# Kernel tuning notes

Measured on AMD Instinct MI355X. Metric: run time of the kernel, lower is better.

## Reference

```python
import jax, jax.numpy as jnp
import numpy as np

GROUP_SIZE = 64  # matches init_kwargs group_size


def setup_inputs() -> dict:
    key = jax.random.key(0)
    k1, k2, k3, k4 = jax.random.split(key, 4)
    B, S, D_in, D_out = 4, 2048, 4096, 4096
    x = jax.random.normal(k1, (B, S, D_in), dtype=jnp.float32)
    # symmetric int8 quantized weights in [-127, 127]
    weight_quant = jax.random.randint(k2, (D_out, D_in), -127, 128, dtype=jnp.int32)
    num_groups = (D_out * D_in) // GROUP_SIZE
    # positive per-group scales (abs_max / 127 of a typical weight group)
    weight_scale = jax.random.uniform(k3, (num_groups,), dtype=jnp.float32,
                                      minval=1e-3, maxval=2e-2)
    bias = jax.random.normal(k4, (D_out,), dtype=jnp.float32) * 0.01
    return {"x": x, "weight_quant": weight_quant,
            "weight_scale": weight_scale, "bias": bias}


def reference(x, weight_quant, weight_scale, bias):
    # Group-wise symmetric dequantization: flatten row-major, scale each
    # contiguous group of GROUP_SIZE elements by its own scale.
    out_f, in_f = weight_quant.shape
    w = weight_quant.astype(jnp.float32).reshape(-1, GROUP_SIZE)  # [num_groups, G]
    w = w * weight_scale[:, None]
    w = w.reshape(out_f, in_f).astype(x.dtype)
    # F.linear(x, W, b) = x @ W^T + b
    return jnp.einsum('bsi,oi->bso', x, w) + bias
```

## Files before the change

### kernel.cpp

```cpp
#include <hip/hip_runtime.h>
#include <stdint.h>


typedef __attribute__((ext_vector_type(8))) short short8;
typedef __attribute__((ext_vector_type(8))) unsigned short ushort8;
typedef __attribute__((ext_vector_type(4))) float f32x4;
typedef __attribute__((ext_vector_type(16))) float f32x16;
typedef __attribute__((ext_vector_type(4))) float float4v;
typedef __attribute__((ext_vector_type(4))) int int4v;

typedef __attribute__((address_space(1))) void g_void;
typedef __attribute__((address_space(3))) void l_void;

__device__ __forceinline__ unsigned short f2bf(float f) {
  union { float f; unsigned int u; } v; v.f = f;
  unsigned int r = v.u + 0x7FFFu + ((v.u >> 16) & 1u);
  return (unsigned short)(r >> 16);
}

__device__ __forceinline__ void async_copy16(const void* g, void* l) {
  __builtin_amdgcn_global_load_lds((const g_void*)g, (l_void*)l, 16, 0, 0);
}

__device__ __forceinline__ void wg_barrier() {
  asm volatile("" ::: "memory");
  __builtin_amdgcn_s_barrier();
  asm volatile("" ::: "memory");
}

#define WAIT_VMCNT(N) asm volatile("s_waitcnt vmcnt(" #N ")" ::: "memory")

__global__ __launch_bounds__(256) void cvt_kernel(
    const float* __restrict__ x, const int* __restrict__ w,
    const float* __restrict__ s, unsigned short* __restrict__ ox,
    unsigned short* __restrict__ ow, int n8x, int n8w, int gx) {
  if ((int)blockIdx.x < gx) {
    int t = blockIdx.x * 256 + threadIdx.x;
    if (t >= n8x) return;
    const float4v* xp = (const float4v*)x + (size_t)t * 2;
    float4v a = xp[0], b = xp[1];
    ushort8 r;
    r[0] = f2bf(a[0]); r[1] = f2bf(a[1]); r[2] = f2bf(a[2]); r[3] = f2bf(a[3]);
    r[4] = f2bf(b[0]); r[5] = f2bf(b[1]); r[6] = f2bf(b[2]); r[7] = f2bf(b[3]);
    *(ushort8*)(ox + (size_t)t * 8) = r;
  } else {
    int t = ((int)blockIdx.x - gx) * 256 + threadIdx.x;
    if (t >= n8w) return;
    const int4v* wp = (const int4v*)w + (size_t)t * 2;
    int4v q0 = wp[0], q1 = wp[1];
    float sc = s[t >> 3];
    ushort8 r;
    r[0] = f2bf((float)q0[0] * sc); r[1] = f2bf((float)q0[1] * sc);
    r[2] = f2bf((float)q0[2] * sc); r[3] = f2bf((float)q0[3] * sc);
    r[4] = f2bf((float)q1[0] * sc); r[5] = f2bf((float)q1[1] * sc);
    r[6] = f2bf((float)q1[2] * sc); r[7] = f2bf((float)q1[3] * sc);
    *(ushort8*)(ow + (size_t)t * 8) = r;
  }
}


#define MF(a, b, c) __builtin_amdgcn_mfma_f32_16x16x32_bf16(a, b, c, 0, 0, 0)

#define LDA(base, mh) do {                              \
    const unsigned char* _p = (base) + aoff + (mh) * 4096; \
    av0 = *(const short8*)(_p);                         \
    av1 = *(const short8*)(_p + 1024);                  \
    av2 = *(const short8*)(_p + 2048);                  \
    av3 = *(const short8*)(_p + 3072);                  \
  } while (0)

#define LDB(base) do {                                  \
    const unsigned char* _p = (base) + boff;            \
    bv0 = *(const short8*)(_p);                         \
    bv1 = *(const short8*)(_p + 1024);                  \
    bv2 = *(const short8*)(_p + 2048);                  \
    bv3 = *(const short8*)(_p + 3072);                  \
  } while (0)

#define MM16(mb) do {                                           \
    acc[(mb)+0][0] = MF(av0, bv0, acc[(mb)+0][0]);              \
    acc[(mb)+0][1] = MF(av0, bv1, acc[(mb)+0][1]);              \
    acc[(mb)+0][2] = MF(av0, bv2, acc[(mb)+0][2]);              \
    acc[(mb)+0][3] = MF(av0, bv3, acc[(mb)+0][3]);              \
    acc[(mb)+1][0] = MF(av1, bv0, acc[(mb)+1][0]);              \
    acc[(mb)+1][1] = MF(av1, bv1, acc[(mb)+1][1]);              \
    acc[(mb)+1][2] = MF(av1, bv2, acc[(mb)+1][2]);              \
    acc[(mb)+1][3] = MF(av1, bv3, acc[(mb)+1][3]);              \
    acc[(mb)+2][0] = MF(av2, bv0, acc[(mb)+2][0]);              \
    acc[(mb)+2][1] = MF(av2, bv1, acc[(mb)+2][1]);              \
    acc[(mb)+2][2] = MF(av2, bv2, acc[(mb)+2][2]);              \
    acc[(mb)+2][3] = MF(av2, bv3, acc[(mb)+2][3]);              \
    acc[(mb)+3][0] = MF(av3, bv0, acc[(mb)+3][0]);              \
    acc[(mb)+3][1] = MF(av3, bv1, acc[(mb)+3][1]);              \
    acc[(mb)+3][2] = MF(av3, bv2, acc[(mb)+3][2]);              \
    acc[(mb)+3][3] = MF(av3, bv3, acc[(mb)+3][3]);              \
  } while (0)

#define PRIO1 __builtin_amdgcn_s_setprio(1)
#define PRIO0 __builtin_amdgcn_s_setprio(0)

__device__ __forceinline__ void stage2(const unsigned short* src, int rstride,
                                       unsigned char* dst) {
  async_copy16(src, dst);
  async_copy16(src + rstride, dst + 8192);
}

__global__ __launch_bounds__(512, 2) void gemm_8p(
    const unsigned short* __restrict__ Xb,
    const unsigned short* __restrict__ Wb,
    const float* __restrict__ bias,
    float* __restrict__ C, int M, int N, int K) {
  __shared__ __align__(16) unsigned char smem[131072];
  const int tid = threadIdx.x;
  const int lane = tid & 63, w = tid >> 6;
  const int wm = w >> 2, wn = w & 3;
  const int l15 = lane & 15;

  const int nbn = N >> 8;
  int bid = blockIdx.x;
  {
    const int nwg = gridDim.x;
    if ((nwg & 7) == 0) bid = (bid & 7) * (nwg >> 3) + (bid >> 3);
  }
  const int m0 = (bid / nbn) << 8;
  const int n0 = (bid % nbn) << 8;

  const int chnk = (((lane >> 4) ^ ((l15 >> 1) & 3)) << 4);
  const int aoff = (wm * 128 + l15) * 64 + chnk;
  const int boff = (wn * 64 + l15) * 64 + chnk;

  const int rl = tid >> 2;
  const int lc = (tid & 3) ^ ((tid >> 3) & 3);
  const unsigned short* pA = Xb + (size_t)(m0 + rl) * K + lc * 8;
  const unsigned short* pB = Wb + (size_t)(n0 + rl) * K + lc * 8;
  const int rstride = K << 7;
  const int wuo = w << 10;

  f32x4 acc[8][4];
#pragma unroll
  for (int i = 0; i < 8; i++)
#pragma unroll
    for (int j = 0; j < 4; j++) acc[i][j] = (f32x4)(0.f);

  const int NT = K >> 6;

  stage2(pA, rstride, smem + wuo);
  stage2(pB, rstride, smem + 65536 + wuo);
  stage2(pA + 32, rstride, smem + 16384 + wuo);
  stage2(pB + 32, rstride, smem + 65536 + 16384 + wuo);
  WAIT_VMCNT(4);
  wg_barrier();

  short8 av0, av1, av2, av3, bv0, bv1, bv2, bv3;

  for (int t = 0; t < NT - 1; ++t) {
    const int p = t & 1;
    const unsigned char* Ab = smem + p * 32768;
    const unsigned char* Bb = smem + 65536 + p * 32768;
    unsigned char* Aq = smem + (p ^ 1) * 32768 + wuo;
    unsigned char* Bq = smem + 65536 + (p ^ 1) * 32768 + wuo;
    const unsigned short* sA = pA + (size_t)(t + 1) * 64;
    const unsigned short* sB = pB + (size_t)(t + 1) * 64;

    LDA(Ab, 0); LDB(Bb);
    stage2(sA, rstride, Aq);
    wg_barrier();
    PRIO1; MM16(0); PRIO0;
    wg_barrier();
    LDA(Ab, 1);
    stage2(sB, rstride, Bq);
    wg_barrier();
    PRIO1; MM16(4); PRIO0;
    WAIT_VMCNT(4);
    wg_barrier();
    LDA(Ab + 16384, 0); LDB(Bb + 16384);
    stage2(sA + 32, rstride, Aq + 16384);
    wg_barrier();
    PRIO1; MM16(0); PRIO0;
    wg_barrier();
    LDA(Ab + 16384, 1);
    stage2(sB + 32, rstride, Bq + 16384);
    wg_barrier();
    PRIO1; MM16(4); PRIO0;
    WAIT_VMCNT(4);
    wg_barrier();
  }

  {
    const int p = (NT - 1) & 1;
    const unsigned char* Ab = smem + p * 32768;
    const unsigned char* Bb = smem + 65536 + p * 32768;
    LDA(Ab, 0); LDB(Bb);
    wg_barrier();
    PRIO1; MM16(0); PRIO0;
    wg_barrier();
    LDA(Ab, 1);
    wg_barrier();
    PRIO1; MM16(4); PRIO0;
    WAIT_VMCNT(0);
    wg_barrier();
    LDA(Ab + 16384, 0); LDB(Bb + 16384);
    wg_barrier();
    PRIO1; MM16(0); PRIO0;
    wg_barrier();
    LDA(Ab + 16384, 1);
    wg_barrier();
    PRIO1; MM16(4); PRIO0;
  }

  const int gm = m0 + wm * 128 + ((lane >> 4) << 2);
  const int gn = n0 + wn * 64 + l15;
  float bvs[4];
#pragma unroll
  for (int g = 0; g < 4; ++g) bvs[g] = bias[gn + g * 16];
#pragma unroll
  for (int mf = 0; mf < 8; ++mf) {
    const size_t rb = (size_t)(gm + mf * 16) * N + gn;
#pragma unroll
    for (int r = 0; r < 4; ++r) {
#pragma unroll
      for (int g = 0; g < 4; ++g)
        C[rb + (size_t)r * N + g * 16] = acc[mf][g][r] + bvs[g];
    }
  }
}

#define BM 128
#define BN 128
#define BK 64

__global__ __launch_bounds__(256) void gemm_fused(
    const float* __restrict__ Xf, const int* __restrict__ Wq,
    const float* __restrict__ Ws, const float* __restrict__ bias,
    float* __restrict__ C, int M, int N, int K) {
  __shared__ unsigned char smem[(BM * BK + BN * BK) * 2];
  const int tid = threadIdx.x;
  const int lane = tid & 63, wid = tid >> 6;
  const int m0 = blockIdx.y * BM, n0 = blockIdx.x * BN;
  const int sr = lane >> 3, fc = (lane & 7) ^ sr;
  const int arow = m0 + wid * 32 + sr, brow = n0 + wid * 32 + sr;
  unsigned char* As = smem;
  unsigned char* Bs = smem + BM * BK * 2;
  unsigned char* stA = As + wid * 4096 + lane * 16;
  unsigned char* stB = Bs + wid * 4096 + lane * 16;
  const int l31 = lane & 31, lh = lane >> 5, le = lane & 7;
  const int wm = (wid & 1) * 64, wn = (wid >> 1) * 64;
  const unsigned char* Aw = As + (wm + l31) * 128;
  const unsigned char* Bw = Bs + (wn + l31) * 128;
  const int Kg = K >> 6;

  f32x16 acc[2][2];
#pragma unroll
  for (int i = 0; i < 2; i++)
#pragma unroll
    for (int j = 0; j < 2; j++) acc[i][j] = (f32x16)(0.f);

  for (int k0 = 0; k0 < K; k0 += BK) {
#pragma unroll
    for (int t = 0; t < 4; t++) {
      const float4v* xa = (const float4v*)(Xf + (size_t)(arow + t * 8) * K + k0 + fc * 8);
      float4v x0 = xa[0], x1 = xa[1];
      ushort8 ra;
      ra[0] = f2bf(x0[0]); ra[1] = f2bf(x0[1]); ra[2] = f2bf(x0[2]); ra[3] = f2bf(x0[3]);
      ra[4] = f2bf(x1[0]); ra[5] = f2bf(x1[1]); ra[6] = f2bf(x1[2]); ra[7] = f2bf(x1[3]);
      *(ushort8*)(stA + t * 1024) = ra;
      const int4v* wq = (const int4v*)(Wq + (size_t)(brow + t * 8) * K + k0 + fc * 8);
      int4v q0 = wq[0], q1 = wq[1];
      float sc = Ws[(size_t)(brow + t * 8) * Kg + (k0 >> 6)];
      ushort8 rb;
      rb[0] = f2bf((float)q0[0] * sc); rb[1] = f2bf((float)q0[1] * sc);
      rb[2] = f2bf((float)q0[2] * sc); rb[3] = f2bf((float)q0[3] * sc);
      rb[4] = f2bf((float)q1[0] * sc); rb[5] = f2bf((float)q1[1] * sc);
      rb[6] = f2bf((float)q1[2] * sc); rb[7] = f2bf((float)q1[3] * sc);
      *(ushort8*)(stB + t * 1024) = rb;
    }
    __syncthreads();
#pragma unroll
    for (int s = 0; s < 4; s++) {
      const int off = ((s + 4 * lh) ^ le) << 4;
      short8 a0 = *(const short8*)(Aw + off);
      short8 a1 = *(const short8*)(Aw + 4096 + off);
      short8 b0 = *(const short8*)(Bw + off);
      short8 b1 = *(const short8*)(Bw + 4096 + off);
      acc[0][0] = __builtin_amdgcn_mfma_f32_32x32x16_bf16(a0, b0, acc[0][0], 0, 0, 0);
      acc[0][1] = __builtin_amdgcn_mfma_f32_32x32x16_bf16(a0, b1, acc[0][1], 0, 0, 0);
      acc[1][0] = __builtin_amdgcn_mfma_f32_32x32x16_bf16(a1, b0, acc[1][0], 0, 0, 0);
      acc[1][1] = __builtin_amdgcn_mfma_f32_32x32x16_bf16(a1, b1, acc[1][1], 0, 0, 0);
    }
    __syncthreads();
  }

  const int gm = m0 + wm + 4 * lh, gn = n0 + wn + l31;
#pragma unroll
  for (int j = 0; j < 2; j++) {
    const int col = gn + j * 32;
    const float bv = bias[col];
#pragma unroll
    for (int i = 0; i < 2; i++) {
      const int rbase = gm + i * 32;
      f32x16 v = acc[i][j];
#pragma unroll
      for (int r = 0; r < 16; r++) {
        const int row = rbase + (r & 3) + 8 * (r >> 2);
        C[(size_t)row * N + col] = v[r] + bv;
      }
    }
  }
}

extern "C" void kernel_launch(void* const* d_in, const int* in_sizes, int n_in,
                              void* d_out, int out_size, void* d_ws, size_t ws_size,
                              hipStream_t stream) {
  const float* x = (const float*)d_in[0];
  const int* wq = (const int*)d_in[1];
  const float* wsc = (const float*)d_in[2];
  const float* bias = (const float*)d_in[3];
  float* out = (float*)d_out;

  const int N = in_sizes[3];
  const int K = in_sizes[1] / N;
  const int M = in_sizes[0] / K;

  const size_t needX = (size_t)M * K * 2;
  const size_t needW = (size_t)N * K * 2;
  const bool big = (M % 256 == 0) && (N % 256 == 0) && (K % 64 == 0) && (K >= 128);

  if (big && ws_size >= needX + needW) {
    unsigned short* Xb = (unsigned short*)d_ws;
    unsigned short* Wb = (unsigned short*)((char*)d_ws + needX);
    const int n8x = (M * K) / 8, n8w = (N * K) / 8;
    const int gx = (n8x + 255) / 256, gw = (n8w + 255) / 256;
    cvt_kernel<<<gx + gw, 256, 0, stream>>>(x, wq, wsc, Xb, Wb, n8x, n8w, gx);
    dim3 grid((M / 256) * (N / 256));
    gemm_8p<<<grid, 512, 0, stream>>>(Xb, Wb, bias, out, M, N, K);
  } else {
    dim3 grid(N / BN, M / BM), block(256);
    gemm_fused<<<grid, block, 0, stream>>>(x, wq, wsc, bias, out, M, N, K);
  }
}
```

Before: 500.6 us.

## Switch GEMM to 32x32x16 MFMA, fewer barriers, grid-stride convert kernel

The main GEMM now uses 32x32x16 bf16 MFMA tiles in place of 16x16x32, with a new LDS read pattern and swizzle. Each K-half loads all of its operands in one batch, and all four async stages are issued up front, which removes half of the workgroup barriers per iteration. The conversion kernel becomes a grid-stride loop over a fixed grid of 1376+688 blocks rather than one block per chunk. The larger MFMA halves the number of instructions and cuts LDS read traffic per flop. In exchange, the epilogue stores become less coalesced and the new wait counts and swizzle must be exactly right.

Result: slower. 579.8 us (+15.8%).

```diff
diff --git a/kernel.cpp b/kernel.cpp
--- a/kernel.cpp
+++ b/kernel.cpp
@@ -35,65 +35,68 @@
     const float* __restrict__ s, unsigned short* __restrict__ ox,
     unsigned short* __restrict__ ow, int n8x, int n8w, int gx) {
   if ((int)blockIdx.x < gx) {
-    int t = blockIdx.x * 256 + threadIdx.x;
-    if (t >= n8x) return;
-    const float4v* xp = (const float4v*)x + (size_t)t * 2;
-    float4v a = xp[0], b = xp[1];
-    ushort8 r;
-    r[0] = f2bf(a[0]); r[1] = f2bf(a[1]); r[2] = f2bf(a[2]); r[3] = f2bf(a[3]);
-    r[4] = f2bf(b[0]); r[5] = f2bf(b[1]); r[6] = f2bf(b[2]); r[7] = f2bf(b[3]);
-    *(ushort8*)(ox + (size_t)t * 8) = r;
+    const int stride = gx * 256;
+    for (int t = blockIdx.x * 256 + threadIdx.x; t < n8x; t += stride) {
+      const float4v* xp = (const float4v*)x + (size_t)t * 2;
+      float4v a = xp[0], b = xp[1];
+      ushort8 r;
+      r[0] = f2bf(a[0]); r[1] = f2bf(a[1]); r[2] = f2bf(a[2]); r[3] = f2bf(a[3]);
+      r[4] = f2bf(b[0]); r[5] = f2bf(b[1]); r[6] = f2bf(b[2]); r[7] = f2bf(b[3]);
+      *(ushort8*)(ox + (size_t)t * 8) = r;
+    }
   } else {
-    int t = ((int)blockIdx.x - gx) * 256 + threadIdx.x;
-    if (t >= n8w) return;
-    const int4v* wp = (const int4v*)w + (size_t)t * 2;
-    int4v q0 = wp[0], q1 = wp[1];
-    float sc = s[t >> 3];
-    ushort8 r;
-    r[0] = f2bf((float)q0[0] * sc); r[1] = f2bf((float)q0[1] * sc);
-    r[2] = f2bf((float)q0[2] * sc); r[3] = f2bf((float)q0[3] * sc);
-    r[4] = f2bf((float)q1[0] * sc); r[5] = f2bf((float)q1[1] * sc);
-    r[6] = f2bf((float)q1[2] * sc); r[7] = f2bf((float)q1[3] * sc);
-    *(ushort8*)(ow + (size_t)t * 8) = r;
-  }
-}
-
-
-#define MF(a, b, c) __builtin_amdgcn_mfma_f32_16x16x32_bf16(a, b, c, 0, 0, 0)
-
-#define LDA(base, mh) do {                              \
-    const unsigned char* _p = (base) + aoff + (mh) * 4096; \
-    av0 = *(const short8*)(_p);                         \
-    av1 = *(const short8*)(_p + 1024);                  \
-    av2 = *(const short8*)(_p + 2048);                  \
-    av3 = *(const short8*)(_p + 3072);                  \
+    const int stride = ((int)gridDim.x - gx) * 256;
+    for (int t = ((int)blockIdx.x - gx) * 256 + threadIdx.x; t < n8w; t += stride) {
+      const int4v* wp = (const int4v*)w + (size_t)t * 2;
+      int4v q0 = wp[0], q1 = wp[1];
+      float sc = s[t >> 3];
+      ushort8 r;
+      r[0] = f2bf((float)q0[0] * sc); r[1] = f2bf((float)q0[1] * sc);
+      r[2] = f2bf((float)q0[2] * sc); r[3] = f2bf((float)q0[3] * sc);
+      r[4] = f2bf((float)q1[0] * sc); r[5] = f2bf((float)q1[1] * sc);
+      r[6] = f2bf((float)q1[2] * sc); r[7] = f2bf((float)q1[3] * sc);
+      *(ushort8*)(ow + (size_t)t * 8) = r;
+    }
+  }
+}
+
+
+#define MF32(a, b, c) __builtin_amdgcn_mfma_f32_32x32x16_bf16(a, b, c, 0, 0, 0)
+
+#define READ12(AU, BU) do {                              \
+    const unsigned char* _a = (AU) + abase;              \
+    const unsigned char* _b = (BU) + bbase;              \
+    a00 = *(const short8*)(_a + ca0);                    \
+    a10 = *(const short8*)(_a + 2048 + ca0);             \
+    a20 = *(const short8*)(_a + 4096 + ca0);             \
+    a30 = *(const short8*)(_a + 6144 + ca0);             \
+    a01 = *(const short8*)(_a + ca1);                    \
+    a11 = *(const short8*)(_a + 2048 + ca1);             \
+    a21 = *(const short8*)(_a + 4096 + ca1);             \
+    a31 = *(const short8*)(_a + 6144 + ca1);             \
+    b00 = *(const short8*)(_b + ca0);                    \
+    b10 = *(const short8*)(_b + 2048 + ca0);             \
+    b01 = *(const short8*)(_b + ca1);                    \
+    b11 = *(const short8*)(_b + 2048 + ca1);             \
   } while (0)
 
-#define LDB(base) do {                                  \
-    const unsigned char* _p = (base) + boff;            \
-    bv0 = *(const short8*)(_p);                         \
-    bv1 = *(const short8*)(_p + 1024);                  \
-    bv2 = *(const short8*)(_p + 2048);                  \
-    bv3 = *(const short8*)(_p + 3072);                  \
-  } while (0)
-
-#define MM16(mb) do {                                           \
-    acc[(mb)+0][0] = MF(av0, bv0, acc[(mb)+0][0]);              \
-    acc[(mb)+0][1] = MF(av0, bv1, acc[(mb)+0][1]);              \
-    acc[(mb)+0][2] = MF(av0, bv2, acc[(mb)+0][2]);              \
-    acc[(mb)+0][3] = MF(av0, bv3, acc[(mb)+0][3]);              \
-    acc[(mb)+1][0] = MF(av1, bv0, acc[(mb)+1][0]);              \
-    acc[(mb)+1][1] = MF(av1, bv1, acc[(mb)+1][1]);              \
-    acc[(mb)+1][2] = MF(av1, bv2, acc[(mb)+1][2]);              \
-    acc[(mb)+1][3] = MF(av1, bv3, acc[(mb)+1][3]);              \
-    acc[(mb)+2][0] = MF(av2, bv0, acc[(mb)+2][0]);              \
-    acc[(mb)+2][1] = MF(av2, bv1, acc[(mb)+2][1]);              \
-    acc[(mb)+2][2] = MF(av2, bv2, acc[(mb)+2][2]);              \
-    acc[(mb)+2][3] = MF(av2, bv3, acc[(mb)+2][3]);              \
-    acc[(mb)+3][0] = MF(av3, bv0, acc[(mb)+3][0]);              \
-    acc[(mb)+3][1] = MF(av3, bv1, acc[(mb)+3][1]);              \
-    acc[(mb)+3][2] = MF(av3, bv2, acc[(mb)+3][2]);              \
-    acc[(mb)+3][3] = MF(av3, bv3, acc[(mb)+3][3]);              \
+#define MFMA16() do {                                    \
+    acc[0][0] = MF32(a00, b00, acc[0][0]);               \
+    acc[1][0] = MF32(a10, b00, acc[1][0]);               \
+    acc[2][0] = MF32(a20, b00, acc[2][0]);               \
+    acc[3][0] = MF32(a30, b00, acc[3][0]);               \
+    acc[0][1] = MF32(a00, b10, acc[0][1]);               \
+    acc[1][1] = MF32(a10, b10, acc[1][1]);               \
+    acc[2][1] = MF32(a20, b10, acc[2][1]);               \
+    acc[3][1] = MF32(a30, b10, acc[3][1]);               \
+    acc[0][0] = MF32(a01, b01, acc[0][0]);               \
+    acc[1][0] = MF32(a11, b01, acc[1][0]);               \
+    acc[2][0] = MF32(a21, b01, acc[2][0]);               \
+    acc[3][0] = MF32(a31, b01, acc[3][0]);               \
+    acc[0][1] = MF32(a01, b11, acc[0][1]);               \
+    acc[1][1] = MF32(a11, b11, acc[1][1]);               \
+    acc[2][1] = MF32(a21, b11, acc[2][1]);               \
+    acc[3][1] = MF32(a31, b11, acc[3][1]);               \
   } while (0)
 
 #define PRIO1 __builtin_amdgcn_s_setprio(1)
@@ -114,7 +117,7 @@
   const int tid = threadIdx.x;
   const int lane = tid & 63, w = tid >> 6;
   const int wm = w >> 2, wn = w & 3;
-  const int l15 = lane & 15;
+  const int l31 = lane & 31, kg = lane >> 5;
 
   const int nbn = N >> 8;
   int bid = blockIdx.x;
@@ -125,9 +128,11 @@
   const int m0 = (bid / nbn) << 8;
   const int n0 = (bid % nbn) << 8;
 
-  const int chnk = (((lane >> 4) ^ ((l15 >> 1) & 3)) << 4);
-  const int aoff = (wm * 128 + l15) * 64 + chnk;
-  const int boff = (wn * 64 + l15) * 64 + chnk;
+  const int xr = (l31 >> 1) & 3;
+  const int ca0 = ((0 + kg) ^ xr) << 4;
+  const int ca1 = ((2 + kg) ^ xr) << 4;
+  const int abase = (wm * 128 + l31) * 64;
+  const int bbase = (wn * 64 + l31) * 64;
 
   const int rl = tid >> 2;
   const int lc = (tid & 3) ^ ((tid >> 3) & 3);
@@ -136,11 +141,11 @@
   const int rstride = K << 7;
   const int wuo = w << 10;
 
-  f32x4 acc[8][4];
-#pragma unroll
-  for (int i = 0; i < 8; i++)
-#pragma unroll
-    for (int j = 0; j < 4; j++) acc[i][j] = (f32x4)(0.f);
+  f32x16 acc[4][2];
+#pragma unroll
+  for (int i = 0; i < 4; i++)
+#pragma unroll
+    for (int j = 0; j < 2; j++) acc[i][j] = (f32x16)(0.f);
 
   const int NT = K >> 6;
 
@@ -151,76 +156,62 @@
   WAIT_VMCNT(4);
   wg_barrier();
 
-  short8 av0, av1, av2, av3, bv0, bv1, bv2, bv3;
+  short8 a00, a10, a20, a30, a01, a11, a21, a31, b00, b10, b01, b11;
 
   for (int t = 0; t < NT - 1; ++t) {
     const int p = t & 1;
-    const unsigned char* Ab = smem + p * 32768;
-    const unsigned char* Bb = smem + 65536 + p * 32768;
+    const unsigned char* Au = smem + p * 32768;
+    const unsigned char* Bu = smem + 65536 + p * 32768;
     unsigned char* Aq = smem + (p ^ 1) * 32768 + wuo;
     unsigned char* Bq = smem + 65536 + (p ^ 1) * 32768 + wuo;
     const unsigned short* sA = pA + (size_t)(t + 1) * 64;
     const unsigned short* sB = pB + (size_t)(t + 1) * 64;
 
-    LDA(Ab, 0); LDB(Bb);
+    READ12(Au, Bu);
     stage2(sA, rstride, Aq);
-    wg_barrier();
-    PRIO1; MM16(0); PRIO0;
-    wg_barrier();
-    LDA(Ab, 1);
     stage2(sB, rstride, Bq);
-    wg_barrier();
-    PRIO1; MM16(4); PRIO0;
-    WAIT_VMCNT(4);
-    wg_barrier();
-    LDA(Ab + 16384, 0); LDB(Bb + 16384);
     stage2(sA + 32, rstride, Aq + 16384);
-    wg_barrier();
-    PRIO1; MM16(0); PRIO0;
-    wg_barrier();
-    LDA(Ab + 16384, 1);
     stage2(sB + 32, rstride, Bq + 16384);
     wg_barrier();
-    PRIO1; MM16(4); PRIO0;
+    PRIO1; MFMA16(); PRIO0;
+    WAIT_VMCNT(8);
+    wg_barrier();
+    READ12(Au + 16384, Bu + 16384);
+    wg_barrier();
+    PRIO1; MFMA16(); PRIO0;
     WAIT_VMCNT(4);
     wg_barrier();
   }
 
   {
     const int p = (NT - 1) & 1;
-    const unsigned char* Ab = smem + p * 32768;
-    const unsigned char* Bb = smem + 65536 + p * 32768;
-    LDA(Ab, 0); LDB(Bb);
-    wg_barrier();
-    PRIO1; MM16(0); PRIO0;
-    wg_barrier();
-    LDA(Ab, 1);
-    wg_barrier();
-    PRIO1; MM16(4); PRIO0;
+    const unsigned char* Au = smem + p * 32768;
+    const unsigned char* Bu = smem + 65536 + p * 32768;
+    READ12(Au, Bu);
+    wg_barrier();
+    PRIO1; MFMA16(); PRIO0;
     WAIT_VMCNT(0);
     wg_barrier();
-    LDA(Ab + 16384, 0); LDB(Bb + 16384);
-    wg_barrier();
-    PRIO1; MM16(0); PRIO0;
-    wg_barrier();
-    LDA(Ab + 16384, 1);
-    wg_barrier();
-    PRIO1; MM16(4); PRIO0;
-  }
-
-  const int gm = m0 + wm * 128 + ((lane >> 4) << 2);
-  const int gn = n0 + wn * 64 + l15;
-  float bvs[4];
-#pragma unroll
-  for (int g = 0; g < 4; ++g) bvs[g] = bias[gn + g * 16];
-#pragma unroll
-  for (int mf = 0; mf < 8; ++mf) {
-    const size_t rb = (size_t)(gm + mf * 16) * N + gn;
-#pragma unroll
-    for (int r = 0; r < 4; ++r) {
-#pragma unroll
-      for (int g = 0; g < 4; ++g)
-        C[rb + (size_t)r * N + g * 16] = acc[mf][g][r] + bvs[g];
+    READ12(Au + 16384, Bu + 16384);
+    wg_barrier();
+    PRIO1; MFMA16(); PRIO0;
+  }
+
+  const int gm = m0 + wm * 128 + 4 * kg;
+  const int gn = n0 + wn * 64 + l31;
+  const float bv0 = bias[gn], bv1 = bias[gn + 32];
+#pragma unroll
+  for (int mt = 0; mt < 4; ++mt) {
+#pragma unroll
+    for (int nt = 0; nt < 2; ++nt) {
+      const float bv = nt ? bv1 : bv0;
+      const int col = gn + nt * 32;
+      f32x16 v = acc[mt][nt];
+#pragma unroll
+      for (int r = 0; r < 16; ++r) {
+        const int row = gm + mt * 32 + (r & 3) + 8 * (r >> 2);
+        C[(size_t)row * N + col] = v[r] + bv;
+      }
     }
   }
 }
@@ -329,7 +320,7 @@
     unsigned short* Xb = (unsigned short*)d_ws;
     unsigned short* Wb = (unsigned short*)((char*)d_ws + needX);
     const int n8x = (M * K) / 8, n8w = (N * K) / 8;
-    const int gx = (n8x + 255) / 256, gw = (n8w + 255) / 256;
+    const int gx = 1376, gw = 688;
     cvt_kernel<<<gx + gw, 256, 0, stream>>>(x, wq, wsc, Xb, Wb, n8x, n8w, gx);
     dim3 grid((M / 256) * (N / 256));
     gemm_8p<<<grid, 512, 0, stream>>>(Xb, Wb, bias, out, M, N, K);
```

## Shrink GEMM tile to 128x256 with BK32 double buffer and grid-stride convert

Applied to the files above, without the earlier changes.

The main bf16 GEMM now uses 128x256 block tiles with a K-step of 32 and a smaller 48 KB shared buffer. Each wave keeps a 64x64 accumulator, and launch bounds ask for 4 blocks per CU, trading per-block data reuse for higher occupancy and more blocks. The pipeline is simpler: async copy of the next tile, then MFMA on the current one, then a full vmcnt wait and barrier each step, so load latency is less hidden. The conversion kernel becomes grid-stride with fixed block counts to cut launch size.

Result: slower. 540.8 us (+8.0%).

```diff
diff --git a/kernel.cpp b/kernel.cpp
--- a/kernel.cpp
+++ b/kernel.cpp
@@ -35,34 +35,36 @@
     const float* __restrict__ s, unsigned short* __restrict__ ox,
     unsigned short* __restrict__ ow, int n8x, int n8w, int gx) {
   if ((int)blockIdx.x < gx) {
-    int t = blockIdx.x * 256 + threadIdx.x;
-    if (t >= n8x) return;
-    const float4v* xp = (const float4v*)x + (size_t)t * 2;
-    float4v a = xp[0], b = xp[1];
-    ushort8 r;
-    r[0] = f2bf(a[0]); r[1] = f2bf(a[1]); r[2] = f2bf(a[2]); r[3] = f2bf(a[3]);
-    r[4] = f2bf(b[0]); r[5] = f2bf(b[1]); r[6] = f2bf(b[2]); r[7] = f2bf(b[3]);
-    *(ushort8*)(ox + (size_t)t * 8) = r;
+    const int stride = gx * 256;
+    for (int t = blockIdx.x * 256 + threadIdx.x; t < n8x; t += stride) {
+      const float4v* xp = (const float4v*)x + (size_t)t * 2;
+      float4v a = xp[0], b = xp[1];
+      ushort8 r;
+      r[0] = f2bf(a[0]); r[1] = f2bf(a[1]); r[2] = f2bf(a[2]); r[3] = f2bf(a[3]);
+      r[4] = f2bf(b[0]); r[5] = f2bf(b[1]); r[6] = f2bf(b[2]); r[7] = f2bf(b[3]);
+      *(ushort8*)(ox + (size_t)t * 8) = r;
+    }
   } else {
-    int t = ((int)blockIdx.x - gx) * 256 + threadIdx.x;
-    if (t >= n8w) return;
-    const int4v* wp = (const int4v*)w + (size_t)t * 2;
-    int4v q0 = wp[0], q1 = wp[1];
-    float sc = s[t >> 3];
-    ushort8 r;
-    r[0] = f2bf((float)q0[0] * sc); r[1] = f2bf((float)q0[1] * sc);
-    r[2] = f2bf((float)q0[2] * sc); r[3] = f2bf((float)q0[3] * sc);
-    r[4] = f2bf((float)q1[0] * sc); r[5] = f2bf((float)q1[1] * sc);
-    r[6] = f2bf((float)q1[2] * sc); r[7] = f2bf((float)q1[3] * sc);
-    *(ushort8*)(ow + (size_t)t * 8) = r;
-  }
-}
-
-
-#define MF(a, b, c) __builtin_amdgcn_mfma_f32_16x16x32_bf16(a, b, c, 0, 0, 0)
-
-#define LDA(base, mh) do {                              \
-    const unsigned char* _p = (base) + aoff + (mh) * 4096; \
+    const int stride = ((int)gridDim.x - gx) * 256;
+    for (int t = ((int)blockIdx.x - gx) * 256 + threadIdx.x; t < n8w; t += stride) {
+      const int4v* wp = (const int4v*)w + (size_t)t * 2;
+      int4v q0 = wp[0], q1 = wp[1];
+      float sc = s[t >> 3];
+      ushort8 r;
+      r[0] = f2bf((float)q0[0] * sc); r[1] = f2bf((float)q0[1] * sc);
+      r[2] = f2bf((float)q0[2] * sc); r[3] = f2bf((float)q0[3] * sc);
+      r[4] = f2bf((float)q1[0] * sc); r[5] = f2bf((float)q1[1] * sc);
+      r[6] = f2bf((float)q1[2] * sc); r[7] = f2bf((float)q1[3] * sc);
+      *(ushort8*)(ow + (size_t)t * 8) = r;
+    }
+  }
+}
+
+
+#define MF16(a, b, c) __builtin_amdgcn_mfma_f32_16x16x32_bf16(a, b, c, 0, 0, 0)
+
+#define LDA(base) do {                                  \
+    const unsigned char* _p = (base) + aoff;            \
     av0 = *(const short8*)(_p);                         \
     av1 = *(const short8*)(_p + 1024);                  \
     av2 = *(const short8*)(_p + 2048);                  \
@@ -77,23 +79,23 @@
     bv3 = *(const short8*)(_p + 3072);                  \
   } while (0)
 
-#define MM16(mb) do {                                           \
-    acc[(mb)+0][0] = MF(av0, bv0, acc[(mb)+0][0]);              \
-    acc[(mb)+0][1] = MF(av0, bv1, acc[(mb)+0][1]);              \
-    acc[(mb)+0][2] = MF(av0, bv2, acc[(mb)+0][2]);              \
-    acc[(mb)+0][3] = MF(av0, bv3, acc[(mb)+0][3]);              \
-    acc[(mb)+1][0] = MF(av1, bv0, acc[(mb)+1][0]);              \
-    acc[(mb)+1][1] = MF(av1, bv1, acc[(mb)+1][1]);              \
-    acc[(mb)+1][2] = MF(av1, bv2, acc[(mb)+1][2]);              \
-    acc[(mb)+1][3] = MF(av1, bv3, acc[(mb)+1][3]);              \
-    acc[(mb)+2][0] = MF(av2, bv0, acc[(mb)+2][0]);              \
-    acc[(mb)+2][1] = MF(av2, bv1, acc[(mb)+2][1]);              \
-    acc[(mb)+2][2] = MF(av2, bv2, acc[(mb)+2][2]);              \
-    acc[(mb)+2][3] = MF(av2, bv3, acc[(mb)+2][3]);              \
-    acc[(mb)+3][0] = MF(av3, bv0, acc[(mb)+3][0]);              \
-    acc[(mb)+3][1] = MF(av3, bv1, acc[(mb)+3][1]);              \
-    acc[(mb)+3][2] = MF(av3, bv2, acc[(mb)+3][2]);              \
-    acc[(mb)+3][3] = MF(av3, bv3, acc[(mb)+3][3]);              \
+#define MM16() do {                                     \
+    acc[0][0] = MF16(av0, bv0, acc[0][0]);              \
+    acc[0][1] = MF16(av0, bv1, acc[0][1]);              \
+    acc[0][2] = MF16(av0, bv2, acc[0][2]);              \
+    acc[0][3] = MF16(av0, bv3, acc[0][3]);              \
+    acc[1][0] = MF16(av1, bv0, acc[1][0]);              \
+    acc[1][1] = MF16(av1, bv1, acc[1][1]);              \
+    acc[1][2] = MF16(av1, bv2, acc[1][2]);              \
+    acc[1][3] = MF16(av1, bv3, acc[1][3]);              \
+    acc[2][0] = MF16(av2, bv0, acc[2][0]);              \
+    acc[2][1] = MF16(av2, bv1, acc[2][1]);              \
+    acc[2][2] = MF16(av2, bv2, acc[2][2]);              \
+    acc[2][3] = MF16(av2, bv3, acc[2][3]);              \
+    acc[3][0] = MF16(av3, bv0, acc[3][0]);              \
+    acc[3][1] = MF16(av3, bv1, acc[3][1]);              \
+    acc[3][2] = MF16(av3, bv2, acc[3][2]);              \
+    acc[3][3] = MF16(av3, bv3, acc[3][3]);              \
   } while (0)
 
 #define PRIO1 __builtin_amdgcn_s_setprio(1)
@@ -105,12 +107,21 @@
   async_copy16(src + rstride, dst + 8192);
 }
 
-__global__ __launch_bounds__(512, 2) void gemm_8p(
+#define TILE(Au, Bu, Aq, Bq, koff) do {                 \
+    async_copy16(pA + (koff), Aq);                      \
+    stage2(pB + (koff), rstride, Bq);                   \
+    LDA(Au); LDB(Bu);                                   \
+    PRIO1; MM16(); PRIO0;                               \
+    WAIT_VMCNT(0);                                      \
+    wg_barrier();                                       \
+  } while (0)
+
+__global__ __launch_bounds__(512, 4) void gemm_8p(
     const unsigned short* __restrict__ Xb,
     const unsigned short* __restrict__ Wb,
     const float* __restrict__ bias,
     float* __restrict__ C, int M, int N, int K) {
-  __shared__ __align__(16) unsigned char smem[131072];
+  __shared__ __align__(16) unsigned char smem[49152];
   const int tid = threadIdx.x;
   const int lane = tid & 63, w = tid >> 6;
   const int wm = w >> 2, wn = w & 3;
@@ -122,11 +133,11 @@
     const int nwg = gridDim.x;
     if ((nwg & 7) == 0) bid = (bid & 7) * (nwg >> 3) + (bid >> 3);
   }
-  const int m0 = (bid / nbn) << 8;
+  const int m0 = (bid / nbn) << 7;
   const int n0 = (bid % nbn) << 8;
 
   const int chnk = (((lane >> 4) ^ ((l15 >> 1) & 3)) << 4);
-  const int aoff = (wm * 128 + l15) * 64 + chnk;
+  const int aoff = (wm * 64 + l15) * 64 + chnk;
   const int boff = (wn * 64 + l15) * 64 + chnk;
 
   const int rl = tid >> 2;
@@ -136,91 +147,52 @@
   const int rstride = K << 7;
   const int wuo = w << 10;
 
-  f32x4 acc[8][4];
-#pragma unroll
-  for (int i = 0; i < 8; i++)
+  const unsigned char* A0 = smem;
+  const unsigned char* A1 = smem + 8192;
+  const unsigned char* B0 = smem + 16384;
+  const unsigned char* B1 = smem + 32768;
+  unsigned char* A0q = smem + wuo;
+  unsigned char* A1q = smem + 8192 + wuo;
+  unsigned char* B0q = smem + 16384 + wuo;
+  unsigned char* B1q = smem + 32768 + wuo;
+
+  f32x4 acc[4][4];
+#pragma unroll
+  for (int i = 0; i < 4; i++)
 #pragma unroll
     for (int j = 0; j < 4; j++) acc[i][j] = (f32x4)(0.f);
 
-  const int NT = K >> 6;
-
-  stage2(pA, rstride, smem + wuo);
-  stage2(pB, rstride, smem + 65536 + wuo);
-  stage2(pA + 32, rstride, smem + 16384 + wuo);
-  stage2(pB + 32, rstride, smem + 65536 + 16384 + wuo);
-  WAIT_VMCNT(4);
+  const int NT = K >> 5;
+
+  async_copy16(pA, A0q);
+  stage2(pB, rstride, B0q);
+  WAIT_VMCNT(0);
   wg_barrier();
 
   short8 av0, av1, av2, av3, bv0, bv1, bv2, bv3;
 
-  for (int t = 0; t < NT - 1; ++t) {
-    const int p = t & 1;
-    const unsigned char* Ab = smem + p * 32768;
-    const unsigned char* Bb = smem + 65536 + p * 32768;
-    unsigned char* Aq = smem + (p ^ 1) * 32768 + wuo;
-    unsigned char* Bq = smem + 65536 + (p ^ 1) * 32768 + wuo;
-    const unsigned short* sA = pA + (size_t)(t + 1) * 64;
-    const unsigned short* sB = pB + (size_t)(t + 1) * 64;
-
-    LDA(Ab, 0); LDB(Bb);
-    stage2(sA, rstride, Aq);
-    wg_barrier();
-    PRIO1; MM16(0); PRIO0;
-    wg_barrier();
-    LDA(Ab, 1);
-    stage2(sB, rstride, Bq);
-    wg_barrier();
-    PRIO1; MM16(4); PRIO0;
-    WAIT_VMCNT(4);
-    wg_barrier();
-    LDA(Ab + 16384, 0); LDB(Bb + 16384);
-    stage2(sA + 32, rstride, Aq + 16384);
-    wg_barrier();
-    PRIO1; MM16(0); PRIO0;
-    wg_barrier();
-    LDA(Ab + 16384, 1);
-    stage2(sB + 32, rstride, Bq + 16384);
-    wg_barrier();
-    PRIO1; MM16(4); PRIO0;
-    WAIT_VMCNT(4);
-    wg_barrier();
-  }
-
-  {
-    const int p = (NT - 1) & 1;
-    const unsigned char* Ab = smem + p * 32768;
-    const unsigned char* Bb = smem + 65536 + p * 32768;
-    LDA(Ab, 0); LDB(Bb);
-    wg_barrier();
-    PRIO1; MM16(0); PRIO0;
-    wg_barrier();
-    LDA(Ab, 1);
-    wg_barrier();
-    PRIO1; MM16(4); PRIO0;
-    WAIT_VMCNT(0);
-    wg_barrier();
-    LDA(Ab + 16384, 0); LDB(Bb + 16384);
-    wg_barrier();
-    PRIO1; MM16(0); PRIO0;
-    wg_barrier();
-    LDA(Ab + 16384, 1);
-    wg_barrier();
-    PRIO1; MM16(4); PRIO0;
-  }
-
-  const int gm = m0 + wm * 128 + ((lane >> 4) << 2);
+  for (int t2 = 0; t2 < (NT >> 1) - 1; ++t2) {
+    const int koff = t2 * 64 + 32;
+    TILE(A0, B0, A1q, B1q, koff);
+    TILE(A1, B1, A0q, B0q, koff + 32);
+  }
+  TILE(A0, B0, A1q, B1q, (NT - 1) * 32);
+  LDA(A1); LDB(B1);
+  PRIO1; MM16(); PRIO0;
+
+  const int gm = m0 + wm * 64 + ((lane >> 4) << 2);
   const int gn = n0 + wn * 64 + l15;
   float bvs[4];
 #pragma unroll
   for (int g = 0; g < 4; ++g) bvs[g] = bias[gn + g * 16];
 #pragma unroll
-  for (int mf = 0; mf < 8; ++mf) {
-    const size_t rb = (size_t)(gm + mf * 16) * N + gn;
+  for (int mt = 0; mt < 4; ++mt) {
+    const size_t rb = (size_t)(gm + mt * 16) * N + gn;
 #pragma unroll
     for (int r = 0; r < 4; ++r) {
 #pragma unroll
-      for (int g = 0; g < 4; ++g)
-        C[rb + (size_t)r * N + g * 16] = acc[mf][g][r] + bvs[g];
+      for (int nt = 0; nt < 4; ++nt)
+        C[rb + (size_t)r * N + nt * 16] = acc[mt][nt][r] + bvs[nt];
     }
   }
 }
@@ -323,15 +295,15 @@
 
   const size_t needX = (size_t)M * K * 2;
   const size_t needW = (size_t)N * K * 2;
-  const bool big = (M % 256 == 0) && (N % 256 == 0) && (K % 64 == 0) && (K >= 128);
+  const bool big = (M % 128 == 0) && (N % 256 == 0) && (K % 64 == 0) && (K >= 128);
 
   if (big && ws_size >= needX + needW) {
     unsigned short* Xb = (unsigned short*)d_ws;
     unsigned short* Wb = (unsigned short*)((char*)d_ws + needX);
     const int n8x = (M * K) / 8, n8w = (N * K) / 8;
-    const int gx = (n8x + 255) / 256, gw = (n8w + 255) / 256;
+    const int gx = 1376, gw = 688;
     cvt_kernel<<<gx + gw, 256, 0, stream>>>(x, wq, wsc, Xb, Wb, n8x, n8w, gx);
-    dim3 grid((M / 256) * (N / 256));
+    dim3 grid((M / 128) * (N / 256));
     gemm_8p<<<grid, 512, 0, stream>>>(Xb, Wb, bias, out, M, N, K);
   } else {
     dim3 grid(N / BN, M / BM), block(256);
```

## Deepen GEMM prefetch to half-tile granularity and grid-stride conversion kernel

Applied to the files above, without the earlier changes.

The GEMM main loop now keeps loads in flight one half-K-tile further ahead, issuing the next tile's second half and the following tile's first half while computing the current one. The wait count rises to allow more outstanding global-to-LDS copies, and a peeled second-to-last iteration handles the pipeline tail. The conversion kernel switches to a grid-stride loop with a fixed block count sized to the device instead of one block per chunk. The deeper prefetch reuses buffer slots more tightly, which risks LDS hazards, and the fixed grid sizes are tuned to this hardware.

After: 518.1 us. +3.5%, slower.

```diff
diff --git a/kernel.cpp b/kernel.cpp
--- a/kernel.cpp
+++ b/kernel.cpp
@@ -35,26 +35,28 @@
     const float* __restrict__ s, unsigned short* __restrict__ ox,
     unsigned short* __restrict__ ow, int n8x, int n8w, int gx) {
   if ((int)blockIdx.x < gx) {
-    int t = blockIdx.x * 256 + threadIdx.x;
-    if (t >= n8x) return;
-    const float4v* xp = (const float4v*)x + (size_t)t * 2;
-    float4v a = xp[0], b = xp[1];
-    ushort8 r;
-    r[0] = f2bf(a[0]); r[1] = f2bf(a[1]); r[2] = f2bf(a[2]); r[3] = f2bf(a[3]);
-    r[4] = f2bf(b[0]); r[5] = f2bf(b[1]); r[6] = f2bf(b[2]); r[7] = f2bf(b[3]);
-    *(ushort8*)(ox + (size_t)t * 8) = r;
+    const int stride = gx * 256;
+    for (int t = blockIdx.x * 256 + threadIdx.x; t < n8x; t += stride) {
+      const float4v* xp = (const float4v*)x + (size_t)t * 2;
+      float4v a = xp[0], b = xp[1];
+      ushort8 r;
+      r[0] = f2bf(a[0]); r[1] = f2bf(a[1]); r[2] = f2bf(a[2]); r[3] = f2bf(a[3]);
+      r[4] = f2bf(b[0]); r[5] = f2bf(b[1]); r[6] = f2bf(b[2]); r[7] = f2bf(b[3]);
+      *(ushort8*)(ox + (size_t)t * 8) = r;
+    }
   } else {
-    int t = ((int)blockIdx.x - gx) * 256 + threadIdx.x;
-    if (t >= n8w) return;
-    const int4v* wp = (const int4v*)w + (size_t)t * 2;
-    int4v q0 = wp[0], q1 = wp[1];
-    float sc = s[t >> 3];
-    ushort8 r;
-    r[0] = f2bf((float)q0[0] * sc); r[1] = f2bf((float)q0[1] * sc);
-    r[2] = f2bf((float)q0[2] * sc); r[3] = f2bf((float)q0[3] * sc);
-    r[4] = f2bf((float)q1[0] * sc); r[5] = f2bf((float)q1[1] * sc);
-    r[6] = f2bf((float)q1[2] * sc); r[7] = f2bf((float)q1[3] * sc);
-    *(ushort8*)(ow + (size_t)t * 8) = r;
+    const int stride = ((int)gridDim.x - gx) * 256;
+    for (int t = ((int)blockIdx.x - gx) * 256 + threadIdx.x; t < n8w; t += stride) {
+      const int4v* wp = (const int4v*)w + (size_t)t * 2;
+      int4v q0 = wp[0], q1 = wp[1];
+      float sc = s[t >> 3];
+      ushort8 r;
+      r[0] = f2bf((float)q0[0] * sc); r[1] = f2bf((float)q0[1] * sc);
+      r[2] = f2bf((float)q0[2] * sc); r[3] = f2bf((float)q0[3] * sc);
+      r[4] = f2bf((float)q1[0] * sc); r[5] = f2bf((float)q1[1] * sc);
+      r[6] = f2bf((float)q1[2] * sc); r[7] = f2bf((float)q1[3] * sc);
+      *(ushort8*)(ow + (size_t)t * 8) = r;
+    }
   }
 }
 
@@ -148,38 +150,73 @@
   stage2(pB, rstride, smem + 65536 + wuo);
   stage2(pA + 32, rstride, smem + 16384 + wuo);
   stage2(pB + 32, rstride, smem + 65536 + 16384 + wuo);
-  WAIT_VMCNT(4);
+  stage2(pA + 64, rstride, smem + 32768 + wuo);
+  stage2(pB + 64, rstride, smem + 65536 + 32768 + wuo);
+  WAIT_VMCNT(8);
   wg_barrier();
 
   short8 av0, av1, av2, av3, bv0, bv1, bv2, bv3;
 
-  for (int t = 0; t < NT - 1; ++t) {
+  for (int t = 0; t < NT - 2; ++t) {
     const int p = t & 1;
     const unsigned char* Ab = smem + p * 32768;
     const unsigned char* Bb = smem + 65536 + p * 32768;
-    unsigned char* Aq = smem + (p ^ 1) * 32768 + wuo;
-    unsigned char* Bq = smem + 65536 + (p ^ 1) * 32768 + wuo;
-    const unsigned short* sA = pA + (size_t)(t + 1) * 64;
-    const unsigned short* sB = pB + (size_t)(t + 1) * 64;
+    unsigned char* Aq1 = smem + (p ^ 1) * 32768 + wuo;
+    unsigned char* Bq1 = smem + 65536 + (p ^ 1) * 32768 + wuo;
+    unsigned char* Aq2 = smem + p * 32768 + wuo;
+    unsigned char* Bq2 = smem + 65536 + p * 32768 + wuo;
+    const unsigned short* sA1 = pA + (size_t)(t + 1) * 64;
+    const unsigned short* sB1 = pB + (size_t)(t + 1) * 64;
 
     LDA(Ab, 0); LDB(Bb);
-    stage2(sA, rstride, Aq);
+    stage2(sA1 + 32, rstride, Aq1 + 16384);
     wg_barrier();
     PRIO1; MM16(0); PRIO0;
     wg_barrier();
     LDA(Ab, 1);
-    stage2(sB, rstride, Bq);
-    wg_barrier();
-    PRIO1; MM16(4); PRIO0;
-    WAIT_VMCNT(4);
+    stage2(sB1 + 32, rstride, Bq1 + 16384);
+    wg_barrier();
+    PRIO1; MM16(4); PRIO0;
+    WAIT_VMCNT(8);
     wg_barrier();
     LDA(Ab + 16384, 0); LDB(Bb + 16384);
-    stage2(sA + 32, rstride, Aq + 16384);
+    stage2(sA1 + 64, rstride, Aq2);
     wg_barrier();
     PRIO1; MM16(0); PRIO0;
     wg_barrier();
     LDA(Ab + 16384, 1);
-    stage2(sB + 32, rstride, Bq + 16384);
+    stage2(sB1 + 64, rstride, Bq2);
+    wg_barrier();
+    PRIO1; MM16(4); PRIO0;
+    WAIT_VMCNT(8);
+    wg_barrier();
+  }
+
+  {
+    const int p = (NT - 2) & 1;
+    const unsigned char* Ab = smem + p * 32768;
+    const unsigned char* Bb = smem + 65536 + p * 32768;
+    unsigned char* Aq1 = smem + (p ^ 1) * 32768 + wuo;
+    unsigned char* Bq1 = smem + 65536 + (p ^ 1) * 32768 + wuo;
+    const unsigned short* sA1 = pA + (size_t)(NT - 1) * 64;
+    const unsigned short* sB1 = pB + (size_t)(NT - 1) * 64;
+
+    LDA(Ab, 0); LDB(Bb);
+    stage2(sA1 + 32, rstride, Aq1 + 16384);
+    wg_barrier();
+    PRIO1; MM16(0); PRIO0;
+    wg_barrier();
+    LDA(Ab, 1);
+    stage2(sB1 + 32, rstride, Bq1 + 16384);
+    wg_barrier();
+    PRIO1; MM16(4); PRIO0;
+    WAIT_VMCNT(8);
+    wg_barrier();
+    LDA(Ab + 16384, 0); LDB(Bb + 16384);
+    wg_barrier();
+    PRIO1; MM16(0); PRIO0;
+    wg_barrier();
+    LDA(Ab + 16384, 1);
     wg_barrier();
     PRIO1; MM16(4); PRIO0;
     WAIT_VMCNT(4);
@@ -329,7 +366,7 @@
     unsigned short* Xb = (unsigned short*)d_ws;
     unsigned short* Wb = (unsigned short*)((char*)d_ws + needX);
     const int n8x = (M * K) / 8, n8w = (N * K) / 8;
-    const int gx = (n8x + 255) / 256, gw = (n8w + 255) / 256;
+    const int gx = 1376, gw = 688;
     cvt_kernel<<<gx + gw, 256, 0, stream>>>(x, wq, wsc, Xb, Wb, n8x, n8w, gx);
     dim3 grid((M / 256) * (N / 256));
     gemm_8p<<<grid, 512, 0, stream>>>(Xb, Wb, bias, out, M, N, K);
```
